# Optimization experiments

Measured on AMD Instinct MI355X. Metric: run time of the kernel, lower is better.

Reference implementation:

```python
import jax, jax.numpy as jnp
import numpy as np

N_HEAD = 16
N_STATE = 1024
NEG_INF = -1e9


def setup_inputs() -> dict:
    key = jax.random.key(0)
    k1, = jax.random.split(key, 1)
    B, S = 4, 2048
    x = jax.random.normal(k1, (B, S, 3 * N_STATE), dtype=jnp.float32)
    # causal attention mask (1 = keep, 0 = masked), broadcast over heads
    attn_mask = jnp.tril(jnp.ones((S, S), dtype=jnp.float32))[None, None, :, :]
    attn_mask = jnp.broadcast_to(attn_mask, (B, 1, S, S))
    return {"x": x, "attn_mask": attn_mask}


def reference(x, attn_mask) -> jnp.ndarray:
    B, S, _ = x.shape
    d_head = N_STATE // N_HEAD
    q = x[:, :, :N_STATE].reshape(B, S, N_HEAD, d_head).transpose(0, 2, 1, 3)  # [B,H,S,D]
    k = x[:, :, N_STATE:2 * N_STATE].reshape(B, S, N_HEAD, d_head).transpose(0, 2, 1, 3)
    v = x[:, :, 2 * N_STATE:].reshape(B, S, N_HEAD, d_head).transpose(0, 2, 1, 3)
    scale = 1.0 / jnp.sqrt(jnp.asarray(d_head, dtype=x.dtype))
    w = jnp.einsum('bhqd,bhkd->bhqk', q, k) * scale           # [B,H,S,S]
    w = attn_mask * w + (1.0 - attn_mask) * NEG_INF
    w = jax.nn.softmax(w, axis=-1)
    # attention_dropout is identity at inference (Keras Dropout, training=False)
    a = jnp.einsum('bhqk,bhkd->bhqd', w, v)                   # [B,H,S,D]
    return a.transpose(0, 2, 1, 3).reshape(B, S, N_STATE)
```

## Files before the change

### kernel.cpp

```cpp
#include <hip/hip_runtime.h>


typedef float  f32x4  __attribute__((ext_vector_type(4)));
typedef short  bf16x8 __attribute__((ext_vector_type(8)));

#define NH      16
#define DH      64
#define SEQ     2048
#define NSTATE  1024
#define ROW3    3072
#define NEG_BIG (-1e9f)
#define QSC     (0.125f * 1.4426950408889634f)
#define WS_NEED (33554432u)

static __device__ __forceinline__ unsigned pk2(float x, float y) {
    unsigned ux = __builtin_bit_cast(unsigned, x);
    unsigned uy = __builtin_bit_cast(unsigned, y);
    ux += 0x7FFFu + ((ux >> 16) & 1u);
    uy += 0x7FFFu + ((uy >> 16) & 1u);
    return __builtin_amdgcn_perm(uy, ux, 0x07060302u);
}
static __device__ __forceinline__ short b1(float x) {
    unsigned u = __builtin_bit_cast(unsigned, x);
    u += 0x7FFFu + ((u >> 16) & 1u);
    return (short)(u >> 16);
}
static __device__ __forceinline__ void async16(const void* g, void* l) {
    __builtin_amdgcn_global_load_lds(
        (const __attribute__((address_space(1))) unsigned*)g,
        (__attribute__((address_space(3))) unsigned*)l, 16, 0, 0);
}

__global__ __launch_bounds__(256)
void qkv_prep(const float* __restrict__ x, short* __restrict__ kbf,
              short* __restrict__ vt) {
    const int tid   = threadIdx.x;
    const int stile = blockIdx.x;
    const int bh    = blockIdx.y;
    const int b = bh >> 4, h = bh & 15;
    const int s0 = stile * 64;

    const float* kg = x + (size_t)b * SEQ * ROW3 + NSTATE + h * DH;
    const float* vg = x + (size_t)b * SEQ * ROW3 + 2 * NSTATE + h * DH;

    __shared__ short T[64 * 66];

    unsigned* kout = (unsigned*)kbf + ((size_t)bh * SEQ + s0) * 32;
#pragma unroll
    for (int j = 0; j < 4; ++j) {
        int idx = tid + 256 * j;
        int s   = idx >> 4;
        int dq  = (idx & 15) * 4;
        float4 v = *(const float4*)(kg + (size_t)(s0 + s) * ROW3 + dq);
        unsigned lo = pk2(v.x, v.y), hi = pk2(v.z, v.w);
        int cp = (dq >> 3) ^ (s & 7);
        unsigned* o = kout + s * 32 + cp * 4 + ((dq & 7) >> 1);
        o[0] = lo; o[1] = hi;
    }
#pragma unroll
    for (int j = 0; j < 4; ++j) {
        int idx = tid + 256 * j;
        int s   = idx >> 4;
        int dq  = (idx & 15) * 4;
        float4 v = *(const float4*)(vg + (size_t)(s0 + s) * ROW3 + dq);
        T[(dq + 0) * 66 + s] = b1(v.x);
        T[(dq + 1) * 66 + s] = b1(v.y);
        T[(dq + 2) * 66 + s] = b1(v.z);
        T[(dq + 3) * 66 + s] = b1(v.w);
    }
    __syncthreads();
    {
        unsigned* vout = (unsigned*)vt + (size_t)bh * DH * (SEQ / 2) + (s0 >> 1);
        int d  = tid >> 2;
        int sc = (tid & 3) * 16;
        unsigned r[8];
#pragma unroll
        for (int k = 0; k < 8; ++k)
            r[k] = *(const unsigned*)&T[d * 66 + sc + k * 2];
        int c0  = sc >> 3;
        int c0p = c0 ^ (d & 7);
        int c1p = (c0 + 1) ^ (d & 7);
        uint4 w0 = {r[0], r[1], r[2], r[3]};
        uint4 w1 = {r[4], r[5], r[6], r[7]};
        *(uint4*)(vout + (size_t)d * (SEQ / 2) + c0p * 4) = w0;
        *(uint4*)(vout + (size_t)d * (SEQ / 2) + c1p * 4) = w1;
    }
}

#define BQ2   64
#define NQB2  (SEQ / BQ2)
#define PST   72

__global__ __launch_bounds__(256, 4)
void mha_core(const float* __restrict__ x, const short* __restrict__ kbf,
              const short* __restrict__ vt, float* __restrict__ out) {
    const int tid  = threadIdx.x;
    const int wave = tid >> 6;
    const int lane = tid & 63;
    const int l16  = lane & 15;
    const int quad = lane >> 4;
    const int sw   = l16 & 7;

    const int pr = blockIdx.x;
    const int bh = blockIdx.y;
    const int b  = bh >> 4;
    const int h  = bh & 15;

    const float* xb = x + (size_t)b * SEQ * ROW3;
    float*       ob = out + (size_t)b * SEQ * NSTATE + h * DH;
    const char*  kgb = (const char*)kbf + (size_t)bh * SEQ * 128;
    const char*  vgb = (const char*)vt + (size_t)bh * DH * SEQ * 2;

    __shared__ __align__(16) short Klds[64 * 64];
    __shared__ __align__(16) short Vlds[64 * 64];
    __shared__ __align__(16) short Plds[4][16 * PST];

    bf16x8 vones;
#pragma unroll
    for (int i = 0; i < 8; ++i) vones[i] = (short)0x3F80;

#pragma unroll 1
    for (int ph = 0; ph < 2; ++ph) {
        const int qblk = ph ? (NQB2 - 1 - pr) : pr;
        const int q0   = qblk * BQ2;
        const int qmin = q0 + wave * 16;
        const int qrow = qmin + l16;

        bf16x8 qf[2];
        {
            const float* qp = xb + (size_t)qrow * ROW3 + h * DH + quad * 8;
#pragma unroll
            for (int f = 0; f < 2; ++f) {
                float4 a = *(const float4*)(qp + 32 * f);
                float4 c = *(const float4*)(qp + 32 * f + 4);
                union { bf16x8 v; unsigned u[4]; } qq;
                qq.u[0] = pk2(a.x * QSC, a.y * QSC);
                qq.u[1] = pk2(a.z * QSC, a.w * QSC);
                qq.u[2] = pk2(c.x * QSC, c.y * QSC);
                qq.u[3] = pk2(c.z * QSC, c.w * QSC);
                qf[f] = qq.v;
            }
        }

        f32x4 o[4];
#pragma unroll
        for (int t = 0; t < 4; ++t) o[t] = (f32x4){0.f, 0.f, 0.f, 0.f};
        f32x4 ol = (f32x4){0.f, 0.f, 0.f, 0.f};

        const int nt = q0 / 64 + 1;
#pragma unroll 1
        for (int it = 0; it < nt; ++it) {
            const int kv0 = it * 64;
            __syncthreads();

            {
                const char* kt = kgb + (size_t)kv0 * 128;
                const char* vtt = vgb + (size_t)kv0 * 2;
#pragma unroll
                for (int j = 0; j < 2; ++j) {
                    int seg = wave * 2 + j;
                    async16(kt + seg * 1024 + lane * 16,
                            (char*)Klds + seg * 1024);
                    int d = seg * 8 + (lane >> 3);
                    async16(vtt + (size_t)d * 4096 + (lane & 7) * 16,
                            (char*)Vlds + seg * 1024);
                }
            }
            __syncthreads();

            bf16x8 kf[4][2], vf[4][2];
#pragma unroll
            for (int t = 0; t < 4; ++t)
#pragma unroll
                for (int f = 0; f < 2; ++f) {
                    int off = (16 * t + l16) * 128 + (((quad + 4 * f) ^ sw) * 16);
                    kf[t][f] = *(const bf16x8*)((const char*)Klds + off);
                    vf[t][f] = *(const bf16x8*)((const char*)Vlds + off);
                }

            f32x4 sc[4];
#pragma unroll
            for (int t = 0; t < 4; ++t) {
                f32x4 c = (f32x4){0.f, 0.f, 0.f, 0.f};
                c = __builtin_amdgcn_mfma_f32_16x16x32_bf16(kf[t][0], qf[0], c, 0, 0, 0);
                c = __builtin_amdgcn_mfma_f32_16x16x32_bf16(kf[t][1], qf[1], c, 0, 0, 0);
                sc[t] = c;
            }
            if (it == nt - 1) {
#pragma unroll
                for (int t = 0; t < 4; ++t)
#pragma unroll
                    for (int r = 0; r < 4; ++r) {
                        int kvg = kv0 + 16 * t + 4 * quad + r;
                        if (kvg > qrow) sc[t][r] = NEG_BIG;
                    }
            }

#pragma unroll
            for (int t = 0; t < 4; ++t)
#pragma unroll
                for (int r = 0; r < 4; ++r)
                    sc[t][r] = __builtin_amdgcn_exp2f(sc[t][r]);

            short* pb = &Plds[wave][0];
#pragma unroll
            for (int t = 0; t < 4; ++t) {
                uint2 pk;
                pk.x = pk2(sc[t][0], sc[t][1]);
                pk.y = pk2(sc[t][2], sc[t][3]);
                *(uint2*)&pb[l16 * PST + 16 * t + 4 * quad] = pk;
            }
            __asm__ volatile("s_waitcnt lgkmcnt(0)" ::: "memory");
            bf16x8 pf0 = *(const bf16x8*)&pb[l16 * PST + quad * 8];
            bf16x8 pf1 = *(const bf16x8*)&pb[l16 * PST + quad * 8 + 32];

#pragma unroll
            for (int t = 0; t < 4; ++t) {
                f32x4 c = o[t];
                c = __builtin_amdgcn_mfma_f32_16x16x32_bf16(pf0, vf[t][0], c, 0, 0, 0);
                c = __builtin_amdgcn_mfma_f32_16x16x32_bf16(pf1, vf[t][1], c, 0, 0, 0);
                o[t] = c;
            }
            ol = __builtin_amdgcn_mfma_f32_16x16x32_bf16(pf0, vones, ol, 0, 0, 0);
            ol = __builtin_amdgcn_mfma_f32_16x16x32_bf16(pf1, vones, ol, 0, 0, 0);
        }

        {
            const int qtop = qmin + 4 * quad;
            float lr[4];
#pragma unroll
            for (int r = 0; r < 4; ++r) lr[r] = 1.0f / ol[r];
#pragma unroll
            for (int t = 0; t < 4; ++t)
#pragma unroll
                for (int r = 0; r < 4; ++r)
                    ob[(size_t)(qtop + r) * NSTATE + 16 * t + l16] = o[t][r] * lr[r];
        }
    }
}

#define BQ      128
#define BK      64
#define NQB     (SEQ / BQ)
#define KST     72
#define VST     72

__global__ __launch_bounds__(512, 4)
void mha_fwd_r4(const float* __restrict__ x, float* __restrict__ out) {
    const int tid  = threadIdx.x;
    const int wave = tid >> 6;
    const int lane = tid & 63;
    const int l16  = lane & 15;
    const int quad = lane >> 4;

    const int pr = blockIdx.x;
    const int bh = blockIdx.y;
    const int b  = bh >> 4;
    const int h  = bh & 15;

    const float* xb    = x + (size_t)b * SEQ * ROW3;
    const float* kbase = xb + NSTATE + h * DH;
    const float* vbase = xb + 2 * NSTATE + h * DH;
    float*       ob    = out + (size_t)b * SEQ * NSTATE + h * DH;

    __shared__ __align__(16) short Klds[BK * KST];
    __shared__ __align__(16) short Vlds[DH * VST];
    __shared__ __align__(16) short Plds[8][16 * PST];

    bf16x8 vones;
#pragma unroll
    for (int i = 0; i < 8; ++i) vones[i] = (short)0x3F80;

#pragma unroll 1
    for (int ph = 0; ph < 2; ++ph) {
        const int qblk = ph ? (NQB - 1 - pr) : pr;
        const int q0   = qblk * BQ;
        const int qmin = q0 + wave * 16;
        const int qrow = qmin + l16;

        bf16x8 qf[2];
        {
            const float* qp = xb + (size_t)qrow * ROW3 + h * DH + quad * 8;
#pragma unroll
            for (int f = 0; f < 2; ++f) {
                float4 a = *(const float4*)(qp + 32 * f);
                float4 c = *(const float4*)(qp + 32 * f + 4);
                union { bf16x8 v; unsigned u[4]; } qq;
                qq.u[0] = pk2(a.x * QSC, a.y * QSC);
                qq.u[1] = pk2(a.z * QSC, a.w * QSC);
                qq.u[2] = pk2(c.x * QSC, c.y * QSC);
                qq.u[3] = pk2(c.z * QSC, c.w * QSC);
                qf[f] = qq.v;
            }
        }

        f32x4 o[4];
#pragma unroll
        for (int t = 0; t < 4; ++t) o[t] = (f32x4){0.f, 0.f, 0.f, 0.f};
        f32x4 ol = (f32x4){0.f, 0.f, 0.f, 0.f};

        const int ntiles = q0 / BK + BQ / BK;
#pragma unroll 1
        for (int it = 0; it < ntiles; ++it) {
            const int kv0 = it * BK;
            __syncthreads();
#pragma unroll
            for (int i = 0; i < 2; ++i) {
                int p  = tid + 512 * i;
                int kv = p >> 4;
                int d  = (p & 15) * 4;
                const float* gp = kbase + (size_t)(kv0 + kv) * ROW3 + d;
                float4 v = *(const float4*)gp;
                uint2 pk;
                pk.x = pk2(v.x, v.y);
                pk.y = pk2(v.z, v.w);
                *(uint2*)&Klds[kv * KST + d] = pk;
            }
#pragma unroll
            for (int i = 0; i < 4; ++i) {
                int idx = tid + 512 * i;
                int d   = idx & 63;
                int kv  = (idx >> 6) * 2;
                const float* gp = vbase + (size_t)(kv0 + kv) * ROW3 + d;
                *(unsigned*)&Vlds[d * VST + kv] = pk2(gp[0], gp[ROW3]);
            }
            __syncthreads();

            if (kv0 > qmin + 15) continue;

            bf16x8 kf[4][2], vf[4][2];
#pragma unroll
            for (int t = 0; t < 4; ++t)
#pragma unroll
                for (int f = 0; f < 2; ++f) {
                    kf[t][f] = *(const bf16x8*)&Klds[(16 * t + l16) * KST + quad * 8 + 32 * f];
                    vf[t][f] = *(const bf16x8*)&Vlds[(16 * t + l16) * VST + quad * 8 + 32 * f];
                }

            f32x4 sc[4];
#pragma unroll
            for (int t = 0; t < 4; ++t) {
                f32x4 c = (f32x4){0.f, 0.f, 0.f, 0.f};
                c = __builtin_amdgcn_mfma_f32_16x16x32_bf16(kf[t][0], qf[0], c, 0, 0, 0);
                c = __builtin_amdgcn_mfma_f32_16x16x32_bf16(kf[t][1], qf[1], c, 0, 0, 0);
                sc[t] = c;
            }
            if (kv0 + BK - 1 > qmin) {
#pragma unroll
                for (int t = 0; t < 4; ++t)
#pragma unroll
                    for (int r = 0; r < 4; ++r) {
                        int kvg = kv0 + 16 * t + 4 * quad + r;
                        if (kvg > qrow) sc[t][r] = NEG_BIG;
                    }
            }
#pragma unroll
            for (int t = 0; t < 4; ++t)
#pragma unroll
                for (int r = 0; r < 4; ++r)
                    sc[t][r] = __builtin_amdgcn_exp2f(sc[t][r]);

            short* pb = &Plds[wave][0];
#pragma unroll
            for (int t = 0; t < 4; ++t) {
                uint2 pk;
                pk.x = pk2(sc[t][0], sc[t][1]);
                pk.y = pk2(sc[t][2], sc[t][3]);
                *(uint2*)&pb[l16 * PST + 16 * t + 4 * quad] = pk;
            }
            __asm__ volatile("s_waitcnt lgkmcnt(0)" ::: "memory");
            bf16x8 pf0 = *(const bf16x8*)&pb[l16 * PST + quad * 8];
            bf16x8 pf1 = *(const bf16x8*)&pb[l16 * PST + quad * 8 + 32];

#pragma unroll
            for (int t = 0; t < 4; ++t) {
                f32x4 c = o[t];
                c = __builtin_amdgcn_mfma_f32_16x16x32_bf16(pf0, vf[t][0], c, 0, 0, 0);
                c = __builtin_amdgcn_mfma_f32_16x16x32_bf16(pf1, vf[t][1], c, 0, 0, 0);
                o[t] = c;
            }
            ol = __builtin_amdgcn_mfma_f32_16x16x32_bf16(pf0, vones, ol, 0, 0, 0);
            ol = __builtin_amdgcn_mfma_f32_16x16x32_bf16(pf1, vones, ol, 0, 0, 0);
        }
        {
            const int qtop = qmin + 4 * quad;
            float lr[4];
#pragma unroll
            for (int r = 0; r < 4; ++r) lr[r] = 1.0f / ol[r];
#pragma unroll
            for (int t = 0; t < 4; ++t)
#pragma unroll
                for (int r = 0; r < 4; ++r)
                    ob[(size_t)(qtop + r) * NSTATE + 16 * t + l16] = o[t][r] * lr[r];
        }
    }
}

extern "C" void kernel_launch(void* const* d_in, const int* in_sizes, int n_in,
                              void* d_out, int out_size, void* d_ws, size_t ws_size,
                              hipStream_t stream) {
    const float* x = (const float*)d_in[0];
    float* out = (float*)d_out;
    if (ws_size >= WS_NEED) {
        short* kbf = (short*)d_ws;
        short* vt  = (short*)((char*)d_ws + WS_NEED / 2);
        hipLaunchKernelGGL(qkv_prep, dim3(SEQ / 64, 4 * NH), dim3(256), 0, stream,
                           x, kbf, vt);
        hipLaunchKernelGGL(mha_core, dim3(NQB2 / 2, 4 * NH), dim3(256), 0, stream,
                           x, kbf, vt, out);
    } else {
        hipLaunchKernelGGL(mha_fwd_r4, dim3(NQB / 2, 4 * NH), dim3(512), 0, stream,
                           x, out);
    }
}
```

Before: 261.6 us.

## Register-prefetch K/V tiles, one q-block per CTA, truncating P packing

The attention core drops the paired-q-block scheme and launches one CTA per q-block, ordered heaviest first, with occupancy raised to six blocks per SM. Async global-to-LDS loads are replaced by register double buffering, where the next K/V tile is loaded into registers while the current tile is computed. The P probabilities are packed to bf16 by truncation instead of round-to-nearest, which lowers accuracy slightly. The prep kernel now writes K with wider 16-byte stores and builds the transposed V from packed pairs of rows through a 32-bit LDS tile. The trade-offs are more register pressure from the prefetch buffers and dependence on the hardware scheduler to balance the causal work.

```diff
diff --git a/kernel.cpp b/kernel.cpp
--- a/kernel.cpp
+++ b/kernel.cpp
@@ -20,15 +20,9 @@
     uy += 0x7FFFu + ((uy >> 16) & 1u);
     return __builtin_amdgcn_perm(uy, ux, 0x07060302u);
 }
-static __device__ __forceinline__ short b1(float x) {
-    unsigned u = __builtin_bit_cast(unsigned, x);
-    u += 0x7FFFu + ((u >> 16) & 1u);
-    return (short)(u >> 16);
-}
-static __device__ __forceinline__ void async16(const void* g, void* l) {
-    __builtin_amdgcn_global_load_lds(
-        (const __attribute__((address_space(1))) unsigned*)g,
-        (__attribute__((address_space(3))) unsigned*)l, 16, 0, 0);
+static __device__ __forceinline__ unsigned pk2t(float x, float y) {
+    return __builtin_amdgcn_perm(__builtin_bit_cast(unsigned, y),
+                                 __builtin_bit_cast(unsigned, x), 0x07060302u);
 }
 
 __global__ __launch_bounds__(256)
@@ -43,43 +37,46 @@
     const float* kg = x + (size_t)b * SEQ * ROW3 + NSTATE + h * DH;
     const float* vg = x + (size_t)b * SEQ * ROW3 + 2 * NSTATE + h * DH;
 
-    __shared__ short T[64 * 66];
+    __shared__ unsigned T2[64 * 33];
 
     unsigned* kout = (unsigned*)kbf + ((size_t)bh * SEQ + s0) * 32;
 #pragma unroll
-    for (int j = 0; j < 4; ++j) {
+    for (int j = 0; j < 2; ++j) {
         int idx = tid + 256 * j;
-        int s   = idx >> 4;
+        int s   = idx >> 3;
+        int dq8 = (idx & 7) * 8;
+        const float* gp = kg + (size_t)(s0 + s) * ROW3 + dq8;
+        float4 a = *(const float4*)gp;
+        float4 c = *(const float4*)(gp + 4);
+        uint4 w;
+        w.x = pk2(a.x, a.y); w.y = pk2(a.z, a.w);
+        w.z = pk2(c.x, c.y); w.w = pk2(c.z, c.w);
+        int cp = (dq8 >> 3) ^ (s & 7);
+        *(uint4*)(kout + s * 32 + cp * 4) = w;
+    }
+#pragma unroll
+    for (int j = 0; j < 2; ++j) {
+        int idx = tid + 256 * j;
+        int s2  = idx >> 4;
         int dq  = (idx & 15) * 4;
-        float4 v = *(const float4*)(kg + (size_t)(s0 + s) * ROW3 + dq);
-        unsigned lo = pk2(v.x, v.y), hi = pk2(v.z, v.w);
-        int cp = (dq >> 3) ^ (s & 7);
-        unsigned* o = kout + s * 32 + cp * 4 + ((dq & 7) >> 1);
-        o[0] = lo; o[1] = hi;
-    }
-#pragma unroll
-    for (int j = 0; j < 4; ++j) {
-        int idx = tid + 256 * j;
-        int s   = idx >> 4;
-        int dq  = (idx & 15) * 4;
-        float4 v = *(const float4*)(vg + (size_t)(s0 + s) * ROW3 + dq);
-        T[(dq + 0) * 66 + s] = b1(v.x);
-        T[(dq + 1) * 66 + s] = b1(v.y);
-        T[(dq + 2) * 66 + s] = b1(v.z);
-        T[(dq + 3) * 66 + s] = b1(v.w);
+        const float* g0 = vg + (size_t)(s0 + 2 * s2) * ROW3 + dq;
+        float4 a = *(const float4*)g0;
+        float4 c = *(const float4*)(g0 + ROW3);
+        T2[(dq + 0) * 33 + s2] = pk2(a.x, c.x);
+        T2[(dq + 1) * 33 + s2] = pk2(a.y, c.y);
+        T2[(dq + 2) * 33 + s2] = pk2(a.z, c.z);
+        T2[(dq + 3) * 33 + s2] = pk2(a.w, c.w);
     }
     __syncthreads();
     {
         unsigned* vout = (unsigned*)vt + (size_t)bh * DH * (SEQ / 2) + (s0 >> 1);
-        int d  = tid >> 2;
-        int sc = (tid & 3) * 16;
+        int d = tid >> 2;
+        int c = tid & 3;
         unsigned r[8];
 #pragma unroll
-        for (int k = 0; k < 8; ++k)
-            r[k] = *(const unsigned*)&T[d * 66 + sc + k * 2];
-        int c0  = sc >> 3;
-        int c0p = c0 ^ (d & 7);
-        int c1p = (c0 + 1) ^ (d & 7);
+        for (int k = 0; k < 8; ++k) r[k] = T2[d * 33 + c * 8 + k];
+        int c0p = (2 * c) ^ (d & 7);
+        int c1p = (2 * c + 1) ^ (d & 7);
         uint4 w0 = {r[0], r[1], r[2], r[3]};
         uint4 w1 = {r[4], r[5], r[6], r[7]};
         *(uint4*)(vout + (size_t)d * (SEQ / 2) + c0p * 4) = w0;
@@ -91,7 +88,7 @@
 #define NQB2  (SEQ / BQ2)
 #define PST   72
 
-__global__ __launch_bounds__(256, 4)
+__global__ __launch_bounds__(256, 6)
 void mha_core(const float* __restrict__ x, const short* __restrict__ kbf,
               const short* __restrict__ vt, float* __restrict__ out) {
     const int tid  = threadIdx.x;
@@ -101,13 +98,13 @@
     const int quad = lane >> 4;
     const int sw   = l16 & 7;
 
-    const int pr = blockIdx.x;
-    const int bh = blockIdx.y;
-    const int b  = bh >> 4;
-    const int h  = bh & 15;
-
-    const float* xb = x + (size_t)b * SEQ * ROW3;
-    float*       ob = out + (size_t)b * SEQ * NSTATE + h * DH;
+    const int qblk = (NQB2 - 1) - blockIdx.x;
+    const int bh   = blockIdx.y;
+    const int b    = bh >> 4;
+    const int h    = bh & 15;
+
+    const float* xb  = x + (size_t)b * SEQ * ROW3;
+    float*       ob  = out + (size_t)b * SEQ * NSTATE + h * DH;
     const char*  kgb = (const char*)kbf + (size_t)bh * SEQ * 128;
     const char*  vgb = (const char*)vt + (size_t)bh * DH * SEQ * 2;
 
@@ -119,123 +116,127 @@
 #pragma unroll
     for (int i = 0; i < 8; ++i) vones[i] = (short)0x3F80;
 
+    const int q0   = qblk * BQ2;
+    const int qmin = q0 + wave * 16;
+    const int qrow = qmin + l16;
+
+    bf16x8 qf[2];
+    {
+        const float* qp = xb + (size_t)qrow * ROW3 + h * DH + quad * 8;
+#pragma unroll
+        for (int f = 0; f < 2; ++f) {
+            float4 a = *(const float4*)(qp + 32 * f);
+            float4 c = *(const float4*)(qp + 32 * f + 4);
+            union { bf16x8 v; unsigned u[4]; } qq;
+            qq.u[0] = pk2(a.x * QSC, a.y * QSC);
+            qq.u[1] = pk2(a.z * QSC, a.w * QSC);
+            qq.u[2] = pk2(c.x * QSC, c.y * QSC);
+            qq.u[3] = pk2(c.z * QSC, c.w * QSC);
+            qf[f] = qq.v;
+        }
+    }
+
+    f32x4 o[4];
+#pragma unroll
+    for (int t = 0; t < 4; ++t) o[t] = (f32x4){0.f, 0.f, 0.f, 0.f};
+    f32x4 ol = (f32x4){0.f, 0.f, 0.f, 0.f};
+
+    const int nt = qblk + 1;
+    const int vin = (tid & 7) * 16;
+    const int vd0 = tid >> 3;
+
+    uint4 kr0, kr1, vr0, vr1;
+    kr0 = *(const uint4*)(kgb + tid * 16);
+    kr1 = *(const uint4*)(kgb + 4096 + tid * 16);
+    vr0 = *(const uint4*)(vgb + (size_t)vd0 * 4096 + vin);
+    vr1 = *(const uint4*)(vgb + (size_t)(32 + vd0) * 4096 + vin);
+
 #pragma unroll 1
-    for (int ph = 0; ph < 2; ++ph) {
-        const int qblk = ph ? (NQB2 - 1 - pr) : pr;
-        const int q0   = qblk * BQ2;
-        const int qmin = q0 + wave * 16;
-        const int qrow = qmin + l16;
-
-        bf16x8 qf[2];
-        {
-            const float* qp = xb + (size_t)qrow * ROW3 + h * DH + quad * 8;
+    for (int it = 0; it < nt; ++it) {
+        __syncthreads();
+        *(uint4*)((char*)Klds + tid * 16)        = kr0;
+        *(uint4*)((char*)Klds + 4096 + tid * 16) = kr1;
+        *(uint4*)((char*)Vlds + tid * 16)        = vr0;
+        *(uint4*)((char*)Vlds + 4096 + tid * 16) = vr1;
+        __syncthreads();
+
+        if (it + 1 < nt) {
+            const char* ktn = kgb + (size_t)(it + 1) * 8192;
+            const char* vtn = vgb + (size_t)(it + 1) * 128;
+            kr0 = *(const uint4*)(ktn + tid * 16);
+            kr1 = *(const uint4*)(ktn + 4096 + tid * 16);
+            vr0 = *(const uint4*)(vtn + (size_t)vd0 * 4096 + vin);
+            vr1 = *(const uint4*)(vtn + (size_t)(32 + vd0) * 4096 + vin);
+        }
+
+        bf16x8 kf[4][2], vf[4][2];
+#pragma unroll
+        for (int t = 0; t < 4; ++t)
 #pragma unroll
             for (int f = 0; f < 2; ++f) {
-                float4 a = *(const float4*)(qp + 32 * f);
-                float4 c = *(const float4*)(qp + 32 * f + 4);
-                union { bf16x8 v; unsigned u[4]; } qq;
-                qq.u[0] = pk2(a.x * QSC, a.y * QSC);
-                qq.u[1] = pk2(a.z * QSC, a.w * QSC);
-                qq.u[2] = pk2(c.x * QSC, c.y * QSC);
-                qq.u[3] = pk2(c.z * QSC, c.w * QSC);
-                qf[f] = qq.v;
-            }
-        }
-
-        f32x4 o[4];
-#pragma unroll
-        for (int t = 0; t < 4; ++t) o[t] = (f32x4){0.f, 0.f, 0.f, 0.f};
-        f32x4 ol = (f32x4){0.f, 0.f, 0.f, 0.f};
-
-        const int nt = q0 / 64 + 1;
-#pragma unroll 1
-        for (int it = 0; it < nt; ++it) {
+                int off = (16 * t + l16) * 128 + (((quad + 4 * f) ^ sw) * 16);
+                kf[t][f] = *(const bf16x8*)((const char*)Klds + off);
+                vf[t][f] = *(const bf16x8*)((const char*)Vlds + off);
+            }
+
+        f32x4 sc[4];
+#pragma unroll
+        for (int t = 0; t < 4; ++t) {
+            f32x4 c = (f32x4){0.f, 0.f, 0.f, 0.f};
+            c = __builtin_amdgcn_mfma_f32_16x16x32_bf16(kf[t][0], qf[0], c, 0, 0, 0);
+            c = __builtin_amdgcn_mfma_f32_16x16x32_bf16(kf[t][1], qf[1], c, 0, 0, 0);
+            sc[t] = c;
+        }
+        if (it == nt - 1) {
             const int kv0 = it * 64;
-            __syncthreads();
-
-            {
-                const char* kt = kgb + (size_t)kv0 * 128;
-                const char* vtt = vgb + (size_t)kv0 * 2;
-#pragma unroll
-                for (int j = 0; j < 2; ++j) {
-                    int seg = wave * 2 + j;
-                    async16(kt + seg * 1024 + lane * 16,
-                            (char*)Klds + seg * 1024);
-                    int d = seg * 8 + (lane >> 3);
-                    async16(vtt + (size_t)d * 4096 + (lane & 7) * 16,
-                            (char*)Vlds + seg * 1024);
+#pragma unroll
+            for (int t = 0; t < 4; ++t)
+#pragma unroll
+                for (int r = 0; r < 4; ++r) {
+                    int kvg = kv0 + 16 * t + 4 * quad + r;
+                    if (kvg > qrow) sc[t][r] = NEG_BIG;
                 }
-            }
-            __syncthreads();
-
-            bf16x8 kf[4][2], vf[4][2];
-#pragma unroll
-            for (int t = 0; t < 4; ++t)
-#pragma unroll
-                for (int f = 0; f < 2; ++f) {
-                    int off = (16 * t + l16) * 128 + (((quad + 4 * f) ^ sw) * 16);
-                    kf[t][f] = *(const bf16x8*)((const char*)Klds + off);
-                    vf[t][f] = *(const bf16x8*)((const char*)Vlds + off);
-                }
-
-            f32x4 sc[4];
-#pragma unroll
-            for (int t = 0; t < 4; ++t) {
-                f32x4 c = (f32x4){0.f, 0.f, 0.f, 0.f};
-                c = __builtin_amdgcn_mfma_f32_16x16x32_bf16(kf[t][0], qf[0], c, 0, 0, 0);
-                c = __builtin_amdgcn_mfma_f32_16x16x32_bf16(kf[t][1], qf[1], c, 0, 0, 0);
-                sc[t] = c;
-            }
-            if (it == nt - 1) {
-#pragma unroll
-                for (int t = 0; t < 4; ++t)
-#pragma unroll
-                    for (int r = 0; r < 4; ++r) {
-                        int kvg = kv0 + 16 * t + 4 * quad + r;
-                        if (kvg > qrow) sc[t][r] = NEG_BIG;
-                    }
-            }
-
-#pragma unroll
-            for (int t = 0; t < 4; ++t)
-#pragma unroll
-                for (int r = 0; r < 4; ++r)
-                    sc[t][r] = __builtin_amdgcn_exp2f(sc[t][r]);
-
-            short* pb = &Plds[wave][0];
-#pragma unroll
-            for (int t = 0; t < 4; ++t) {
-                uint2 pk;
-                pk.x = pk2(sc[t][0], sc[t][1]);
-                pk.y = pk2(sc[t][2], sc[t][3]);
-                *(uint2*)&pb[l16 * PST + 16 * t + 4 * quad] = pk;
-            }
-            __asm__ volatile("s_waitcnt lgkmcnt(0)" ::: "memory");
-            bf16x8 pf0 = *(const bf16x8*)&pb[l16 * PST + quad * 8];
-            bf16x8 pf1 = *(const bf16x8*)&pb[l16 * PST + quad * 8 + 32];
-
-#pragma unroll
-            for (int t = 0; t < 4; ++t) {
-                f32x4 c = o[t];
-                c = __builtin_amdgcn_mfma_f32_16x16x32_bf16(pf0, vf[t][0], c, 0, 0, 0);
-                c = __builtin_amdgcn_mfma_f32_16x16x32_bf16(pf1, vf[t][1], c, 0, 0, 0);
-                o[t] = c;
-            }
-            ol = __builtin_amdgcn_mfma_f32_16x16x32_bf16(pf0, vones, ol, 0, 0, 0);
-            ol = __builtin_amdgcn_mfma_f32_16x16x32_bf16(pf1, vones, ol, 0, 0, 0);
-        }
-
-        {
-            const int qtop = qmin + 4 * quad;
-            float lr[4];
-#pragma unroll
-            for (int r = 0; r < 4; ++r) lr[r] = 1.0f / ol[r];
-#pragma unroll
-            for (int t = 0; t < 4; ++t)
-#pragma unroll
-                for (int r = 0; r < 4; ++r)
-                    ob[(size_t)(qtop + r) * NSTATE + 16 * t + l16] = o[t][r] * lr[r];
-        }
+        }
+
+#pragma unroll
+        for (int t = 0; t < 4; ++t)
+#pragma unroll
+            for (int r = 0; r < 4; ++r)
+                sc[t][r] = __builtin_amdgcn_exp2f(sc[t][r]);
+
+        short* pb = &Plds[wave][0];
+#pragma unroll
+        for (int t = 0; t < 4; ++t) {
+            uint2 pk;
+            pk.x = pk2t(sc[t][0], sc[t][1]);
+            pk.y = pk2t(sc[t][2], sc[t][3]);
+            *(uint2*)&pb[l16 * PST + 16 * t + 4 * quad] = pk;
+        }
+        __asm__ volatile("s_waitcnt lgkmcnt(0)" ::: "memory");
+        bf16x8 pf0 = *(const bf16x8*)&pb[l16 * PST + quad * 8];
+        bf16x8 pf1 = *(const bf16x8*)&pb[l16 * PST + quad * 8 + 32];
+
+#pragma unroll
+        for (int t = 0; t < 4; ++t) {
+            f32x4 c = o[t];
+            c = __builtin_amdgcn_mfma_f32_16x16x32_bf16(pf0, vf[t][0], c, 0, 0, 0);
+            c = __builtin_amdgcn_mfma_f32_16x16x32_bf16(pf1, vf[t][1], c, 0, 0, 0);
+            o[t] = c;
+        }
+        ol = __builtin_amdgcn_mfma_f32_16x16x32_bf16(pf0, vones, ol, 0, 0, 0);
+        ol = __builtin_amdgcn_mfma_f32_16x16x32_bf16(pf1, vones, ol, 0, 0, 0);
+    }
+
+    {
+        const int qtop = qmin + 4 * quad;
+        float lr[4];
+#pragma unroll
+        for (int r = 0; r < 4; ++r) lr[r] = 1.0f / ol[r];
+#pragma unroll
+        for (int t = 0; t < 4; ++t)
+#pragma unroll
+            for (int r = 0; r < 4; ++r)
+                ob[(size_t)(qtop + r) * NSTATE + 16 * t + l16] = o[t][r] * lr[r];
     }
 }
 
@@ -406,7 +407,7 @@
         short* vt  = (short*)((char*)d_ws + WS_NEED / 2);
         hipLaunchKernelGGL(qkv_prep, dim3(SEQ / 64, 4 * NH), dim3(256), 0, stream,
                            x, kbf, vt);
-        hipLaunchKernelGGL(mha_core, dim3(NQB2 / 2, 4 * NH), dim3(256), 0, stream,
+        hipLaunchKernelGGL(mha_core, dim3(NQB2, 4 * NH), dim3(256), 0, stream,
                            x, kbf, vt, out);
     } else {
         hipLaunchKernelGGL(mha_fwd_r4, dim3(NQB / 2, 4 * NH), dim3(512), 0, stream,
```

Result: slower. 597.8 us (+128.5%).
